# Kernel tuning notes

Measured on AMD Instinct MI355X. Metric: run time of the kernel, lower is better.

Reference implementation:

```python
import jax, jax.numpy as jnp
import numpy as np


def setup_inputs() -> dict:
    key = jax.random.key(0)
    k1, k2, k3 = jax.random.split(key, 3)
    x = jax.random.normal(k1, (8, 2048, 512), dtype=jnp.float32)
    codebook = jax.random.normal(k2, (8192, 512), dtype=jnp.float32)
    values = jax.random.normal(k3, (8192, 512), dtype=jnp.float32)
    return {"x": x, "codebook": codebook, "values": values}


def reference(x, codebook, values):
    # VectorQuantize: nearest codebook entry under squared L2 distance.
    # dist(b,n,k) = ||x_bn||^2 - 2 x_bn . e_k + ||e_k||^2
    x_sq = jnp.sum(x * x, axis=-1, keepdims=True)            # [b, n, 1]
    e_sq = jnp.sum(codebook * codebook, axis=-1)             # [k]
    dots = jnp.einsum('bnd,kd->bnk', x, codebook)            # [b, n, k] (GEMM)
    memory_indices = jnp.argmin(x_sq - 2.0 * dots + e_sq, axis=-1)  # [b, n]
    # Irregular gather into the memory/value table.
    memories = values[memory_indices]                        # [b, n, dim_memory]
    return memories
```

## Files before the change

kernel.cpp:

```cpp
#include <hip/hip_runtime.h>
#include <hip/hip_bf16.h>


#define D      512
#define M      16384
#define NCODE  8192
#define NSTEP  16
#define ATILEG 131072
#define BTILEG 65536

typedef float f32x4  __attribute__((ext_vector_type(4)));
typedef short bf16x8 __attribute__((ext_vector_type(8)));

#define KMAX 0xFFFFFFFFFFFFFFFFull

__device__ __forceinline__ void gload16(const __hip_bfloat16* g, __hip_bfloat16* l) {
  __builtin_amdgcn_global_load_lds(
      (const __attribute__((address_space(1))) void*)g,
      (__attribute__((address_space(3))) void*)l, 16, 0, 0);
}

__device__ __forceinline__ unsigned long long score_key(float sc, int code) {
  unsigned int u = __float_as_uint(sc);
  unsigned int su = u ^ ((unsigned int)((int)u >> 31) | 0x80000000u);
  return ((unsigned long long)su << 32) | (unsigned int)code;
}

__device__ __forceinline__ void kins2(unsigned long long k,
                                      unsigned long long& k1, unsigned long long& k2) {
  if (k < k1) { k2 = k1; k1 = k; }
  else if (k < k2) { k2 = k; }
}

__device__ __forceinline__ void kins4(unsigned long long k,
    unsigned long long& k0, unsigned long long& k1,
    unsigned long long& k2, unsigned long long& k3) {
  if (k < k0)      { k3 = k2; k2 = k1; k1 = k0; k0 = k; }
  else if (k < k1) { k3 = k2; k2 = k1; k1 = k; }
  else if (k < k2) { k3 = k2; k2 = k; }
  else if (k < k3) { k3 = k; }
}

__global__ __launch_bounds__(256)
void prep256(const float* __restrict__ src, __hip_bfloat16* __restrict__ dst) {
  __shared__ __hip_bfloat16 tile[256][72];
  const int tid = threadIdx.x;
  const int c = blockIdx.x & 7, t = blockIdx.x >> 3;
  const float* srow = src + (size_t)t * 256 * D;
  __hip_bfloat16* dbase = dst + (size_t)t * ATILEG;

#pragma unroll
  for (int j = 0; j < 8; ++j) {
    int f = tid + j * 256;
    int row = f >> 3, k16l = f & 7;
    const float4* p = (const float4*)(srow + (size_t)row * D + c * 64 + k16l * 8);
    float4 v0 = p[0], v1 = p[1];
    float vv[8] = {v0.x, v0.y, v0.z, v0.w, v1.x, v1.y, v1.z, v1.w};
    union { bf16x8 v; unsigned short u[8]; } pk;
#pragma unroll
    for (int e = 0; e < 8; ++e) {
      __hip_bfloat16 h = __float2bfloat16(vv[e]);
      pk.u[e] = *(unsigned short*)&h;
    }
    *(bf16x8*)&tile[row][k16l * 8] = pk.v;
  }
  __syncthreads();
#pragma unroll
  for (int j = 0; j < 8; ++j) {
    int g = tid + j * 256;
    int row = g & 255, k16l = g >> 8;
    bf16x8 v = *(const bf16x8*)&tile[row][k16l * 8];
    *(bf16x8*)(dbase + ((size_t)(c * 8 + k16l) * 256 + row) * 8) = v;
  }
}

__global__ __launch_bounds__(256)
void prep128(const float* __restrict__ src, __hip_bfloat16* __restrict__ dst) {
  __shared__ __hip_bfloat16 tile[128][72];
  const int tid = threadIdx.x;
  const int c = blockIdx.x & 7, t = blockIdx.x >> 3;
  const float* srow = src + (size_t)t * 128 * D;
  __hip_bfloat16* dbase = dst + (size_t)t * BTILEG;

#pragma unroll
  for (int j = 0; j < 4; ++j) {
    int f = tid + j * 256;
    int row = f >> 3, k16l = f & 7;
    const float4* p = (const float4*)(srow + (size_t)row * D + c * 64 + k16l * 8);
    float4 v0 = p[0], v1 = p[1];
    float vv[8] = {v0.x, v0.y, v0.z, v0.w, v1.x, v1.y, v1.z, v1.w};
    union { bf16x8 v; unsigned short u[8]; } pk;
#pragma unroll
    for (int e = 0; e < 8; ++e) {
      __hip_bfloat16 h = __float2bfloat16(vv[e]);
      pk.u[e] = *(unsigned short*)&h;
    }
    *(bf16x8*)&tile[row][k16l * 8] = pk.v;
  }
  __syncthreads();
#pragma unroll
  for (int j = 0; j < 4; ++j) {
    int g = tid + j * 256;
    int row = g & 127, k16l = g >> 7;
    bf16x8 v = *(const bf16x8*)&tile[row][k16l * 8];
    *(bf16x8*)(dbase + ((size_t)(c * 8 + k16l) * 128 + row) * 8) = v;
  }
}

__global__ __launch_bounds__(256)
void rowsumsq(const float* __restrict__ src, float* __restrict__ dst, int nrows) {
  int gw = (blockIdx.x * 256 + threadIdx.x) >> 6;
  if (gw >= nrows) return;
  int lane = threadIdx.x & 63;
  const float4* s4 = (const float4*)(src + (size_t)gw * D);
  float s = 0.f;
#pragma unroll
  for (int i = 0; i < 2; ++i) {
    float4 v = s4[lane + i * 64];
    s += v.x * v.x + v.y * v.y + v.z * v.z + v.w * v.w;
  }
#pragma unroll
  for (int off = 32; off > 0; off >>= 1) s += __shfl_down(s, off, 64);
  if (lane == 0) dst[gw] = s;
}

__global__ __launch_bounds__(256, 2)
void vq_gemm2b(const __hip_bfloat16* __restrict__ Apack,
               const __hip_bfloat16* __restrict__ Bpack,
               const float* __restrict__ e_sq,
               ulonglong2* __restrict__ cand2) {
  __shared__ __hip_bfloat16 As[2][1024 * 8];
  __shared__ __hip_bfloat16 Bs[2][512 * 8];

  const int tid = threadIdx.x;
  const int w = tid >> 6, l = tid & 63;
  const int wr = w >> 1, wc = w & 1;
  const int lr = l & 15, lh = l >> 4;

  const int bid = blockIdx.x;
  const int xcd = bid & 7, idx = bid >> 3;
  const int mt = xcd * 8 + (idx & 7);
  const int ct = idx >> 3;

  const __hip_bfloat16* Abase = Apack + (size_t)mt * ATILEG;
  const __hip_bfloat16* Bbase = Bpack + (size_t)ct * BTILEG;

  f32x4 acc[4][8] = {};

#define STAGE(buf, t)                                                          \
  do {                                                                         \
    _Pragma("unroll")                                                          \
    for (int i = 0; i < 4; ++i)                                                \
      gload16(Abase + ((size_t)(t) * 1024 + tid + i * 256) * 8,                \
              As[(buf)] + (size_t)(tid + i * 256) * 8);                        \
    _Pragma("unroll")                                                          \
    for (int i = 0; i < 2; ++i)                                                \
      gload16(Bbase + ((size_t)(t) * 512 + tid + i * 256) * 8,                 \
              Bs[(buf)] + (size_t)(tid + i * 256) * 8);                        \
  } while (0)

#define COMPUTE(buf)                                                           \
  do {                                                                         \
    const bf16x8* Ag = (const bf16x8*)As[(buf)];                               \
    const bf16x8* Bg = (const bf16x8*)Bs[(buf)];                               \
    const int kb = lh;                                                         \
    bf16x8 a[8], b[4];                                                         \
    _Pragma("unroll")                                                          \
    for (int nc = 0; nc < 4; ++nc) b[nc] = Bg[kb * 128 + wc * 64 + nc * 16 + lr]; \
    _Pragma("unroll")                                                          \
    for (int m = 0; m < 8; ++m)   a[m] = Ag[kb * 256 + wr * 128 + m * 16 + lr];   \
    _Pragma("unroll")                                                          \
    for (int nc = 0; nc < 4; ++nc)                                             \
      _Pragma("unroll")                                                        \
      for (int m = 0; m < 8; ++m)                                              \
        acc[nc][m] = __builtin_amdgcn_mfma_f32_16x16x32_bf16(b[nc], a[m],      \
                                                             acc[nc][m], 0, 0, 0); \
  } while (0)

  STAGE(0, 0);
  __syncthreads();

#pragma unroll 1
  for (int t = 0; t < NSTEP - 1; ++t) {
    const int cur = t & 1;
    STAGE(cur ^ 1, t + 1);
    COMPUTE(cur);
    __syncthreads();
  }
  COMPUTE((NSTEP - 1) & 1);
#undef STAGE
#undef COMPUTE

  const int col0 = ct * 128 + wc * 64;
  float es[4][4];
#pragma unroll
  for (int nc = 0; nc < 4; ++nc) {
    float4 e4 = *(const float4*)&e_sq[col0 + nc * 16 + lh * 4];
    es[nc][0] = e4.x; es[nc][1] = e4.y; es[nc][2] = e4.z; es[nc][3] = e4.w;
  }
#pragma unroll
  for (int m = 0; m < 8; ++m) {
    unsigned long long k1 = KMAX, k2 = KMAX;
#pragma unroll
    for (int nc = 0; nc < 4; ++nc)
#pragma unroll
      for (int q = 0; q < 4; ++q) {
        int code = col0 + nc * 16 + lh * 4 + q;
        kins2(score_key(es[nc][q] - 2.0f * acc[nc][m][q], code), k1, k2);
      }
#pragma unroll
    for (int s = 16; s <= 32; s <<= 1) {
      unsigned long long o1 = __shfl_xor(k1, s, 64);
      unsigned long long o2 = __shfl_xor(k2, s, 64);
      kins2(o1, k1, k2);
      kins2(o2, k1, k2);
    }
    if (lh == 0) {
      int gRow = mt * 256 + wr * 128 + m * 16 + lr;
      cand2[(size_t)gRow * 128 + ct * 2 + wc] = make_ulonglong2(k1, k2);
    }
  }
}

__global__ __launch_bounds__(256)
void vq_merge4(const float* __restrict__ x, const float* __restrict__ cb,
               const float* __restrict__ values, const float* __restrict__ e_sq,
               const ulonglong2* __restrict__ cand2, float* __restrict__ out) {
  int row = blockIdx.x * 4 + (threadIdx.x >> 6);
  int l = threadIdx.x & 63;

  unsigned long long k0 = KMAX, k1 = KMAX, k2 = KMAX, k3 = KMAX;
  const ulonglong2* base = cand2 + (size_t)row * 128;
#pragma unroll
  for (int u = 0; u < 2; ++u) {
    ulonglong2 e = base[l + 64 * u];
    kins4(e.x, k0, k1, k2, k3);
    kins4(e.y, k0, k1, k2, k3);
  }
#pragma unroll
  for (int s = 1; s < 64; s <<= 1) {
    unsigned long long o0 = __shfl_xor(k0, s, 64), o1 = __shfl_xor(k1, s, 64);
    unsigned long long o2 = __shfl_xor(k2, s, 64), o3 = __shfl_xor(k3, s, 64);
    kins4(o0, k0, k1, k2, k3); kins4(o1, k0, k1, k2, k3);
    kins4(o2, k0, k1, k2, k3); kins4(o3, k0, k1, k2, k3);
  }
  int i0 = (int)(k0 & 8191), i1 = (int)(k1 & 8191);
  int i2 = (int)(k2 & 8191), i3 = (int)(k3 & 8191);

  const float4* xr = (const float4*)(x + (size_t)row * D);
  const float4* c0 = (const float4*)(cb + (size_t)i0 * D);
  const float4* c1 = (const float4*)(cb + (size_t)i1 * D);
  const float4* c2 = (const float4*)(cb + (size_t)i2 * D);
  const float4* c3 = (const float4*)(cb + (size_t)i3 * D);
  float xsq = 0.f, t0 = 0.f, t1 = 0.f, t2 = 0.f, t3 = 0.f;
#pragma unroll
  for (int u = 0; u < 2; ++u) {
    float4 xv = xr[l + 64 * u];
    float4 a = c0[l + 64 * u], b = c1[l + 64 * u];
    float4 c = c2[l + 64 * u], e = c3[l + 64 * u];
    xsq += xv.x * xv.x + xv.y * xv.y + xv.z * xv.z + xv.w * xv.w;
    t0 += xv.x * a.x + xv.y * a.y + xv.z * a.z + xv.w * a.w;
    t1 += xv.x * b.x + xv.y * b.y + xv.z * b.z + xv.w * b.w;
    t2 += xv.x * c.x + xv.y * c.y + xv.z * c.z + xv.w * c.w;
    t3 += xv.x * e.x + xv.y * e.y + xv.z * e.z + xv.w * e.w;
  }
#pragma unroll
  for (int s = 1; s < 64; s <<= 1) {
    xsq += __shfl_xor(xsq, s, 64);
    t0 += __shfl_xor(t0, s, 64); t1 += __shfl_xor(t1, s, 64);
    t2 += __shfl_xor(t2, s, 64); t3 += __shfl_xor(t3, s, 64);
  }
  float D0 = xsq - 2.0f * t0 + e_sq[i0];
  float D1 = xsq - 2.0f * t1 + e_sq[i1];
  float D2 = xsq - 2.0f * t2 + e_sq[i2];
  float D3 = xsq - 2.0f * t3 + e_sq[i3];
  float bdist = D0; int best = i0;
  if (D1 < bdist || (D1 == bdist && i1 < best)) { bdist = D1; best = i1; }
  if (D2 < bdist || (D2 == bdist && i2 < best)) { bdist = D2; best = i2; }
  if (D3 < bdist || (D3 == bdist && i3 < best)) { bdist = D3; best = i3; }

  const float4* vsrc = (const float4*)(values + (size_t)best * D);
  float4* dst = (float4*)(out + (size_t)row * D);
  dst[l] = vsrc[l];
  dst[l + 64] = vsrc[l + 64];
}

extern "C" void kernel_launch(void* const* d_in, const int* in_sizes, int n_in,
                              void* d_out, int out_size, void* d_ws, size_t ws_size,
                              hipStream_t stream) {
  const float* x      = (const float*)d_in[0];
  const float* cb     = (const float*)d_in[1];
  const float* values = (const float*)d_in[2];
  float* out = (float*)d_out;

  const size_t A_BYTES = (size_t)M * 512 * 2;
  const size_t B_BYTES = (size_t)NCODE * 512 * 2;
  const size_t C_BYTES = (size_t)M * 128 * 16;

  char* base = (char*)d_ws;
  __hip_bfloat16* Apack = (__hip_bfloat16*)base;
  __hip_bfloat16* Bpack = (__hip_bfloat16*)(base + A_BYTES);
  ulonglong2* cand2 = (ulonglong2*)(base + A_BYTES + B_BYTES);
  float* e_sq = (float*)(base + A_BYTES + B_BYTES + C_BYTES);

  prep256<<<(M / 256) * 8, 256, 0, stream>>>(x, Apack);
  prep128<<<(NCODE / 128) * 8, 256, 0, stream>>>(cb, Bpack);
  rowsumsq<<<NCODE / 4, 256, 0, stream>>>(cb, e_sq, NCODE);
  vq_gemm2b<<<(M / 256) * (NCODE / 128), 256, 0, stream>>>(
      Apack, Bpack, e_sq, cand2);
  vq_merge4<<<M / 4, 256, 0, stream>>>(x, cb, values, e_sq, cand2, out);
}
```

Measured before the change: 798.0 us.

## Keep A tile resident in LDS and stream codebook from global per wave

Replaces the double-buffered 256x128 tiled GEMM with a persistent kernel of 256 blocks. Each block loads a 128-row bf16 A tile (128 KB) into LDS once, and each of its 8 waves streams its own 512-code slice of the codebook straight from global memory into registers, keeping a running top-2 per row. This cuts the candidate buffer from 128 to 16 entries per row and stores the packed operands in the output buffer instead of the workspace. In exchange, B is read from global without LDS sharing, a single 512-thread block per CU may leave latency poorly hidden, and reusing d_out as scratch relies on the merge kernel finishing each row's reads before it is overwritten.

```diff
diff --git a/kernel.cpp b/kernel.cpp
--- a/kernel.cpp
+++ b/kernel.cpp
@@ -5,20 +5,13 @@
 #define D      512
 #define M      16384
 #define NCODE  8192
-#define NSTEP  16
-#define ATILEG 131072
-#define BTILEG 65536
+#define KSTEPS 16
+#define NCH    16
 
 typedef float f32x4  __attribute__((ext_vector_type(4)));
 typedef short bf16x8 __attribute__((ext_vector_type(8)));
 
 #define KMAX 0xFFFFFFFFFFFFFFFFull
-
-__device__ __forceinline__ void gload16(const __hip_bfloat16* g, __hip_bfloat16* l) {
-  __builtin_amdgcn_global_load_lds(
-      (const __attribute__((address_space(1))) void*)g,
-      (__attribute__((address_space(3))) void*)l, 16, 0, 0);
-}
 
 __device__ __forceinline__ unsigned long long score_key(float sc, int code) {
   unsigned int u = __float_as_uint(sc);
@@ -42,68 +35,74 @@
 }
 
 __global__ __launch_bounds__(256)
-void prep256(const float* __restrict__ src, __hip_bfloat16* __restrict__ dst) {
-  __shared__ __hip_bfloat16 tile[256][72];
+void prep_tile(const float* __restrict__ src, __hip_bfloat16* __restrict__ dst) {
+  __shared__ __hip_bfloat16 tile[128][136];
   const int tid = threadIdx.x;
-  const int c = blockIdx.x & 7, t = blockIdx.x >> 3;
-  const float* srow = src + (size_t)t * 256 * D;
-  __hip_bfloat16* dbase = dst + (size_t)t * ATILEG;
-
-#pragma unroll
-  for (int j = 0; j < 8; ++j) {
-    int f = tid + j * 256;
-    int row = f >> 3, k16l = f & 7;
-    const float4* p = (const float4*)(srow + (size_t)row * D + c * 64 + k16l * 8);
-    float4 v0 = p[0], v1 = p[1];
-    float vv[8] = {v0.x, v0.y, v0.z, v0.w, v1.x, v1.y, v1.z, v1.w};
-    union { bf16x8 v; unsigned short u[8]; } pk;
-#pragma unroll
-    for (int e = 0; e < 8; ++e) {
-      __hip_bfloat16 h = __float2bfloat16(vv[e]);
-      pk.u[e] = *(unsigned short*)&h;
-    }
-    *(bf16x8*)&tile[row][k16l * 8] = pk.v;
-  }
-  __syncthreads();
-#pragma unroll
-  for (int j = 0; j < 8; ++j) {
-    int g = tid + j * 256;
-    int row = g & 255, k16l = g >> 8;
-    bf16x8 v = *(const bf16x8*)&tile[row][k16l * 8];
-    *(bf16x8*)(dbase + ((size_t)(c * 8 + k16l) * 256 + row) * 8) = v;
+  const float* srow = src + (size_t)blockIdx.x * 128 * D;
+  __hip_bfloat16* dbase = dst + (size_t)blockIdx.x * 65536;
+
+#pragma unroll 1
+  for (int c = 0; c < 4; ++c) {
+    __syncthreads();
+#pragma unroll
+    for (int j = 0; j < 8; ++j) {
+      int f = tid + j * 256;
+      int row = f >> 4, k16l = f & 15;
+      const float4* p = (const float4*)(srow + (size_t)row * D + c * 128 + k16l * 8);
+      float4 v0 = p[0], v1 = p[1];
+      float vv[8] = {v0.x, v0.y, v0.z, v0.w, v1.x, v1.y, v1.z, v1.w};
+      union { bf16x8 v; unsigned short u[8]; } pk;
+#pragma unroll
+      for (int e = 0; e < 8; ++e) {
+        __hip_bfloat16 h = __float2bfloat16(vv[e]);
+        pk.u[e] = *(unsigned short*)&h;
+      }
+      *(bf16x8*)&tile[row][k16l * 8] = pk.v;
+    }
+    __syncthreads();
+#pragma unroll
+    for (int j = 0; j < 8; ++j) {
+      int g = tid + j * 256;
+      int row = g & 127, k16l = g >> 7;
+      bf16x8 v = *(const bf16x8*)&tile[row][k16l * 8];
+      *(bf16x8*)(dbase + ((size_t)(c * 16 + k16l) * 128 + row) * 8) = v;
+    }
   }
 }
 
 __global__ __launch_bounds__(256)
-void prep128(const float* __restrict__ src, __hip_bfloat16* __restrict__ dst) {
-  __shared__ __hip_bfloat16 tile[128][72];
+void prep_bstream(const float* __restrict__ src, __hip_bfloat16* __restrict__ dst) {
+  __shared__ __hip_bfloat16 tile[128][136];
   const int tid = threadIdx.x;
-  const int c = blockIdx.x & 7, t = blockIdx.x >> 3;
+  const int t = blockIdx.x;
   const float* srow = src + (size_t)t * 128 * D;
-  __hip_bfloat16* dbase = dst + (size_t)t * BTILEG;
-
-#pragma unroll
-  for (int j = 0; j < 4; ++j) {
-    int f = tid + j * 256;
-    int row = f >> 3, k16l = f & 7;
-    const float4* p = (const float4*)(srow + (size_t)row * D + c * 64 + k16l * 8);
-    float4 v0 = p[0], v1 = p[1];
-    float vv[8] = {v0.x, v0.y, v0.z, v0.w, v1.x, v1.y, v1.z, v1.w};
-    union { bf16x8 v; unsigned short u[8]; } pk;
-#pragma unroll
-    for (int e = 0; e < 8; ++e) {
-      __hip_bfloat16 h = __float2bfloat16(vv[e]);
-      pk.u[e] = *(unsigned short*)&h;
-    }
-    *(bf16x8*)&tile[row][k16l * 8] = pk.v;
-  }
-  __syncthreads();
-#pragma unroll
-  for (int j = 0; j < 4; ++j) {
-    int g = tid + j * 256;
-    int row = g & 127, k16l = g >> 7;
-    bf16x8 v = *(const bf16x8*)&tile[row][k16l * 8];
-    *(bf16x8*)(dbase + ((size_t)(c * 8 + k16l) * 128 + row) * 8) = v;
+
+#pragma unroll 1
+  for (int c = 0; c < 4; ++c) {
+    __syncthreads();
+#pragma unroll
+    for (int j = 0; j < 8; ++j) {
+      int f = tid + j * 256;
+      int row = f >> 4, k16l = f & 15;
+      const float4* p = (const float4*)(srow + (size_t)row * D + c * 128 + k16l * 8);
+      float4 v0 = p[0], v1 = p[1];
+      float vv[8] = {v0.x, v0.y, v0.z, v0.w, v1.x, v1.y, v1.z, v1.w};
+      union { bf16x8 v; unsigned short u[8]; } pk;
+#pragma unroll
+      for (int e = 0; e < 8; ++e) {
+        __hip_bfloat16 h = __float2bfloat16(vv[e]);
+        pk.u[e] = *(unsigned short*)&h;
+      }
+      *(bf16x8*)&tile[row][k16l * 8] = pk.v;
+    }
+    __syncthreads();
+#pragma unroll
+    for (int j = 0; j < 8; ++j) {
+      int g = tid + j * 256;
+      int row = g & 127, k16l = g >> 7;
+      bf16x8 v = *(const bf16x8*)&tile[row][k16l * 8];
+      *(bf16x8*)(dst + (((size_t)(c * 16 + k16l) * NCODE) + t * 128 + row) * 8) = v;
+    }
   }
 }
 
@@ -124,116 +123,107 @@
   if (lane == 0) dst[gw] = s;
 }
 
-__global__ __launch_bounds__(256, 2)
-void vq_gemm2b(const __hip_bfloat16* __restrict__ Apack,
+__global__ __launch_bounds__(512, 1)
+void vq_stream(const __hip_bfloat16* __restrict__ Apack,
                const __hip_bfloat16* __restrict__ Bpack,
                const float* __restrict__ e_sq,
                ulonglong2* __restrict__ cand2) {
-  __shared__ __hip_bfloat16 As[2][1024 * 8];
-  __shared__ __hip_bfloat16 Bs[2][512 * 8];
+  extern __shared__ __hip_bfloat16 A_l[];
 
   const int tid = threadIdx.x;
   const int w = tid >> 6, l = tid & 63;
-  const int wr = w >> 1, wc = w & 1;
   const int lr = l & 15, lh = l >> 4;
 
   const int bid = blockIdx.x;
-  const int xcd = bid & 7, idx = bid >> 3;
-  const int mt = xcd * 8 + (idx & 7);
-  const int ct = idx >> 3;
-
-  const __hip_bfloat16* Abase = Apack + (size_t)mt * ATILEG;
-  const __hip_bfloat16* Bbase = Bpack + (size_t)ct * BTILEG;
-
-  f32x4 acc[4][8] = {};
-
-#define STAGE(buf, t)                                                          \
-  do {                                                                         \
-    _Pragma("unroll")                                                          \
-    for (int i = 0; i < 4; ++i)                                                \
-      gload16(Abase + ((size_t)(t) * 1024 + tid + i * 256) * 8,                \
-              As[(buf)] + (size_t)(tid + i * 256) * 8);                        \
-    _Pragma("unroll")                                                          \
-    for (int i = 0; i < 2; ++i)                                                \
-      gload16(Bbase + ((size_t)(t) * 512 + tid + i * 256) * 8,                 \
-              Bs[(buf)] + (size_t)(tid + i * 256) * 8);                        \
-  } while (0)
-
-#define COMPUTE(buf)                                                           \
-  do {                                                                         \
-    const bf16x8* Ag = (const bf16x8*)As[(buf)];                               \
-    const bf16x8* Bg = (const bf16x8*)Bs[(buf)];                               \
-    const int kb = lh;                                                         \
-    bf16x8 a[8], b[4];                                                         \
-    _Pragma("unroll")                                                          \
-    for (int nc = 0; nc < 4; ++nc) b[nc] = Bg[kb * 128 + wc * 64 + nc * 16 + lr]; \
-    _Pragma("unroll")                                                          \
-    for (int m = 0; m < 8; ++m)   a[m] = Ag[kb * 256 + wr * 128 + m * 16 + lr];   \
-    _Pragma("unroll")                                                          \
-    for (int nc = 0; nc < 4; ++nc)                                             \
-      _Pragma("unroll")                                                        \
-      for (int m = 0; m < 8; ++m)                                              \
-        acc[nc][m] = __builtin_amdgcn_mfma_f32_16x16x32_bf16(b[nc], a[m],      \
-                                                             acc[nc][m], 0, 0, 0); \
-  } while (0)
-
-  STAGE(0, 0);
+  const int xcd = bid & 7, i = bid >> 3;
+  const int ch = xcd & 1;
+  const int mt = (xcd >> 1) * 32 + i;
+
+  {
+    const float4* src = (const float4*)(Apack + (size_t)mt * 65536);
+    float4* dst = (float4*)A_l;
+#pragma unroll
+    for (int j = 0; j < 16; ++j) dst[tid + j * 512] = src[tid + j * 512];
+  }
   __syncthreads();
 
+  const bf16x8* Ag = (const bf16x8*)A_l;
+  const int cbase = ch * 4096 + w * 512;
+
+  unsigned long long rk1[8], rk2[8];
+#pragma unroll
+  for (int m = 0; m < 8; ++m) { rk1[m] = KMAX; rk2[m] = KMAX; }
+
 #pragma unroll 1
-  for (int t = 0; t < NSTEP - 1; ++t) {
-    const int cur = t & 1;
-    STAGE(cur ^ 1, t + 1);
-    COMPUTE(cur);
-    __syncthreads();
-  }
-  COMPUTE((NSTEP - 1) & 1);
-#undef STAGE
-#undef COMPUTE
-
-  const int col0 = ct * 128 + wc * 64;
-  float es[4][4];
-#pragma unroll
-  for (int nc = 0; nc < 4; ++nc) {
-    float4 e4 = *(const float4*)&e_sq[col0 + nc * 16 + lh * 4];
-    es[nc][0] = e4.x; es[nc][1] = e4.y; es[nc][2] = e4.z; es[nc][3] = e4.w;
-  }
-#pragma unroll
-  for (int m = 0; m < 8; ++m) {
-    unsigned long long k1 = KMAX, k2 = KMAX;
-#pragma unroll
-    for (int nc = 0; nc < 4; ++nc)
+  for (int j = 0; j < NCH; ++j) {
+    const int c0 = cbase + j * 32;
+    f32x4 acc[2][8] = {};
+
+    bf16x8 nb0 = *(const bf16x8*)(Bpack + ((size_t)lh * NCODE + c0 + lr) * 8);
+    bf16x8 nb1 = *(const bf16x8*)(Bpack + ((size_t)lh * NCODE + c0 + 16 + lr) * 8);
+
+#pragma unroll 1
+    for (int t = 0; t < KSTEPS; ++t) {
+      bf16x8 b0 = nb0, b1 = nb1;
+      if (t + 1 < KSTEPS) {
+        const size_t kg = (size_t)(4 * (t + 1) + lh) * NCODE;
+        nb0 = *(const bf16x8*)(Bpack + (kg + c0 + lr) * 8);
+        nb1 = *(const bf16x8*)(Bpack + (kg + c0 + 16 + lr) * 8);
+      }
+      const int ka = (4 * t + lh) * 128;
+      bf16x8 a[8];
+#pragma unroll
+      for (int m = 0; m < 8; ++m) a[m] = Ag[ka + m * 16 + lr];
+#pragma unroll
+      for (int m = 0; m < 8; ++m) {
+        acc[0][m] = __builtin_amdgcn_mfma_f32_16x16x32_bf16(b0, a[m], acc[0][m], 0, 0, 0);
+        acc[1][m] = __builtin_amdgcn_mfma_f32_16x16x32_bf16(b1, a[m], acc[1][m], 0, 0, 0);
+      }
+    }
+
+    float4 es0 = *(const float4*)&e_sq[c0 + lh * 4];
+    float4 es1 = *(const float4*)&e_sq[c0 + 16 + lh * 4];
+    float e0v[4] = {es0.x, es0.y, es0.z, es0.w};
+    float e1v[4] = {es1.x, es1.y, es1.z, es1.w};
+#pragma unroll
+    for (int m = 0; m < 8; ++m) {
+      unsigned long long k1 = KMAX, k2 = KMAX;
 #pragma unroll
       for (int q = 0; q < 4; ++q) {
-        int code = col0 + nc * 16 + lh * 4 + q;
-        kins2(score_key(es[nc][q] - 2.0f * acc[nc][m][q], code), k1, k2);
-      }
-#pragma unroll
-    for (int s = 16; s <= 32; s <<= 1) {
-      unsigned long long o1 = __shfl_xor(k1, s, 64);
-      unsigned long long o2 = __shfl_xor(k2, s, 64);
-      kins2(o1, k1, k2);
-      kins2(o2, k1, k2);
-    }
-    if (lh == 0) {
-      int gRow = mt * 256 + wr * 128 + m * 16 + lr;
-      cand2[(size_t)gRow * 128 + ct * 2 + wc] = make_ulonglong2(k1, k2);
+        kins2(score_key(e0v[q] - 2.0f * acc[0][m][q], c0 + lh * 4 + q), k1, k2);
+        kins2(score_key(e1v[q] - 2.0f * acc[1][m][q], c0 + 16 + lh * 4 + q), k1, k2);
+      }
+#pragma unroll
+      for (int s = 16; s <= 32; s <<= 1) {
+        unsigned long long o1 = __shfl_xor(k1, s, 64);
+        unsigned long long o2 = __shfl_xor(k2, s, 64);
+        kins2(o1, k1, k2);
+        kins2(o2, k1, k2);
+      }
+      kins2(k1, rk1[m], rk2[m]);
+      kins2(k2, rk1[m], rk2[m]);
+    }
+  }
+
+  if (lh == 0) {
+#pragma unroll
+    for (int m = 0; m < 8; ++m) {
+      int row = mt * 128 + m * 16 + lr;
+      cand2[(size_t)row * 16 + ch * 8 + w] = make_ulonglong2(rk1[m], rk2[m]);
     }
   }
 }
 
 __global__ __launch_bounds__(256)
-void vq_merge4(const float* __restrict__ x, const float* __restrict__ cb,
-               const float* __restrict__ values, const float* __restrict__ e_sq,
-               const ulonglong2* __restrict__ cand2, float* __restrict__ out) {
+void vq_merge16(const float* __restrict__ x, const float* __restrict__ cb,
+                const float* __restrict__ values, const float* __restrict__ e_sq,
+                const ulonglong2* __restrict__ cand2, float* __restrict__ out) {
   int row = blockIdx.x * 4 + (threadIdx.x >> 6);
   int l = threadIdx.x & 63;
 
   unsigned long long k0 = KMAX, k1 = KMAX, k2 = KMAX, k3 = KMAX;
-  const ulonglong2* base = cand2 + (size_t)row * 128;
-#pragma unroll
-  for (int u = 0; u < 2; ++u) {
-    ulonglong2 e = base[l + 64 * u];
+  if (l < 16) {
+    ulonglong2 e = cand2[(size_t)row * 16 + l];
     kins4(e.x, k0, k1, k2, k3);
     kins4(e.y, k0, k1, k2, k3);
   }
@@ -294,19 +284,19 @@
   float* out = (float*)d_out;
 
   const size_t A_BYTES = (size_t)M * 512 * 2;
-  const size_t B_BYTES = (size_t)NCODE * 512 * 2;
-  const size_t C_BYTES = (size_t)M * 128 * 16;
-
-  char* base = (char*)d_ws;
-  __hip_bfloat16* Apack = (__hip_bfloat16*)base;
-  __hip_bfloat16* Bpack = (__hip_bfloat16*)(base + A_BYTES);
-  ulonglong2* cand2 = (ulonglong2*)(base + A_BYTES + B_BYTES);
-  float* e_sq = (float*)(base + A_BYTES + B_BYTES + C_BYTES);
-
-  prep256<<<(M / 256) * 8, 256, 0, stream>>>(x, Apack);
-  prep128<<<(NCODE / 128) * 8, 256, 0, stream>>>(cb, Bpack);
+  __hip_bfloat16* Apack = (__hip_bfloat16*)d_out;
+  __hip_bfloat16* Bpack = (__hip_bfloat16*)((char*)d_out + A_BYTES);
+
+  ulonglong2* cand2 = (ulonglong2*)d_ws;
+  float* e_sq = (float*)((char*)d_ws + (size_t)M * 16 * 16);
+
+  const int LDS_GEMM = 131072;
+  (void)hipFuncSetAttribute(reinterpret_cast<const void*>(vq_stream),
+                            hipFuncAttributeMaxDynamicSharedMemorySize, LDS_GEMM);
+
+  prep_tile<<<M / 128, 256, 0, stream>>>(x, Apack);
+  prep_bstream<<<NCODE / 128, 256, 0, stream>>>(cb, Bpack);
   rowsumsq<<<NCODE / 4, 256, 0, stream>>>(cb, e_sq, NCODE);
-  vq_gemm2b<<<(M / 256) * (NCODE / 128), 256, 0, stream>>>(
-      Apack, Bpack, e_sq, cand2);
-  vq_merge4<<<M / 4, 256, 0, stream>>>(x, cb, values, e_sq, cand2, out);
-}
+  vq_stream<<<256, 512, LDS_GEMM, stream>>>(Apack, Bpack, e_sq, cand2);
+  vq_merge16<<<M / 4, 256, 0, stream>>>(x, cb, values, e_sq, cand2, out);
+}
```

Measured after the change: 920.8 us. 1.15x slower.
